# Performance work log

Measured on AMD Instinct MI355X. Metric: run time of the kernel, lower is better.

The kernel has to match this reference:

```python
import jax, jax.numpy as jnp
import numpy as np
import math

E = 8; K = 2; H_FF = 2048; HEADS = 4; COLLAB_STEPS = 2
AUX_W = 0.01; Z_W = 0.001; DROP_W = 0.001; CAP = 1.25; EPS = 1e-6


def _rms(x, w):
    return x * jax.lax.rsqrt(jnp.mean(x * x, -1, keepdims=True) + EPS) * w


def setup_inputs() -> dict:
    key = jax.random.key(0)
    ks = jax.random.split(key, 16)
    D = 768
    f = lambda k, shape: jax.random.normal(k, shape, jnp.float32) * 0.02
    return dict(
        x=jax.random.normal(ks[0], (4, 2048, D), jnp.float32),
        gate_w=f(ks[1], (E, D)),
        w13=f(ks[2], (E, 2 * H_FF, D)),
        w2=f(ks[3], (E, D, H_FF)),
        in_proj_w=f(ks[4], (3 * D, D)),
        in_proj_b=f(ks[5], (3 * D,)),
        out_w=f(ks[6], (D, D)),
        out_b=f(ks[7], (D,)),
        norm1_w=jnp.ones((D,), jnp.float32),
        norm2_w=jnp.ones((D,), jnp.float32),
        ffn_w1=f(ks[8], (D, D)),
        ffn_w2=f(ks[9], (D, D)),
        mediator=f(ks[10], (1, 1, D)),
        fuse_gate_w=f(ks[11], (1, D)),
        fuse_gate_b=jnp.zeros((1,), jnp.float32),
        o_proj_w=f(ks[12], (D, D)),
    )


def reference(x, gate_w, w13, w2, in_proj_w, in_proj_b, out_w, out_b,
              norm1_w, norm2_w, ffn_w1, ffn_w2, mediator,
              fuse_gate_w, fuse_gate_b, o_proj_w):
    B, T, D = x.shape
    N = B * T
    NK = N * K
    xf = x.reshape(N, D).astype(jnp.float32)

    # ---- router (fp32) ----
    logits = xf @ gate_w.T                                  # [N,E]
    topk_vals, topk_idx = jax.lax.top_k(logits, K)          # [N,K]
    topk_probs = jax.nn.softmax(topk_vals, -1)
    router_probs = jax.nn.softmax(logits, -1)
    assign = jnp.zeros((N, E), jnp.float32).at[jnp.arange(N)[:, None], topk_idx].add(topk_probs)
    balance = (router_probs.mean(0) * assign.mean(0)).sum() * E
    z = jax.nn.logsumexp(logits, -1)
    aux = AUX_W * balance + Z_W * (z * z).mean()

    # ---- capacity-limited dispatch (sort by expert, prio-desc within expert) ----
    C = 1 << int(math.ceil(math.log2(math.ceil(NK / E * CAP))))  # static
    x_exp = jnp.repeat(xf, K, axis=0)                       # [NK,D]
    te = topk_idx.reshape(-1)
    prio = topk_vals.reshape(-1)
    order = jnp.lexsort((-prio, te))                        # expert asc, prio desc
    se = te[order]
    counts = jnp.bincount(te, length=E)
    starts = jnp.concatenate([jnp.zeros(1, counts.dtype), jnp.cumsum(counts)[:-1]])
    pos = jnp.arange(NK) - starts[se]                       # rank within expert
    keep_s = pos < C                                        # top-C by router logit kept
    slot = se * C + jnp.minimum(pos, C - 1)
    slot_w = jnp.where(keep_s, slot, E * C)                 # dropped -> scratch row
    buf = jnp.zeros((E * C + 1, D), jnp.float32).at[slot_w].set(x_exp[order])
    buf = buf[:E * C].reshape(E, C, D)

    # ---- experts: ReasoningFeedForward, n_reasoning_steps=1, alpha=1 ----
    gu = jnp.einsum('ecd,ehd->ech', 2.0 * buf, w13)         # [E,C,2H]
    gate_h, up = jnp.split(gu, 2, axis=-1)
    y = buf + jnp.einsum('ech,edh->ecd', jax.nn.silu(gate_h) * up, w2)
    y_flat = y.reshape(E * C, D)
    y_sorted = jnp.where(keep_s[:, None], y_flat[slot], 0.0)
    expert_out = jnp.zeros((NK, D), jnp.float32).at[order].set(y_sorted)
    keep_mask = jnp.zeros((NK,), bool).at[order].set(keep_s)
    aux = aux + DROP_W * (1.0 - keep_s.astype(jnp.float32).mean())  # drop penalty

    km = keep_mask.reshape(N, K)
    expert_states = expert_out.reshape(N, K, D) * km[..., None]
    tp = topk_probs * km
    denom = tp.sum(-1, keepdims=True)
    ok = denom > 0
    weights = jnp.where(ok, tp / jnp.where(ok, denom, 1.0), 0.0)

    # ---- collaboration: mediator token + R rounds of MHA + FFN ----
    tokens = jnp.concatenate([expert_states, jnp.broadcast_to(mediator, (N, 1, D))], 1)  # [N,K+1,D]
    kpm = jnp.concatenate([~km, jnp.zeros((N, 1), bool)], 1)
    bias = jnp.where(kpm, -1e9, 0.0)[:, None, None, :]      # [N,1,1,L]
    dh = D // HEADS
    scale = 1.0 / math.sqrt(dh)
    L = K + 1
    for _ in range(COLLAB_STEPS):
        qkv = tokens @ in_proj_w.T + in_proj_b
        q, k, v = jnp.split(qkv, 3, -1)
        q = q.reshape(N, L, HEADS, dh)
        k = k.reshape(N, L, HEADS, dh)
        v = v.reshape(N, L, HEADS, dh)
        s = jnp.einsum('nqhd,nkhd->nhqk', q, k) * scale + bias
        a = jax.nn.softmax(s, -1)
        o = jnp.einsum('nhqk,nkhd->nqhd', a, v).reshape(N, L, D) @ out_w.T + out_b
        tokens = _rms(tokens + o, norm1_w)
        tokens = tokens + jax.nn.gelu(_rms(tokens, norm2_w) @ ffn_w1.T, approximate=False) @ ffn_w2.T

    med = tokens[:, -1]
    ref = tokens[:, :-1]
    agg = (ref * weights[..., None]).sum(1)
    g = jax.nn.sigmoid(med @ fuse_gate_w.T + fuse_gate_b)   # [N,1]
    fused = (g * med + (1.0 - g) * agg) @ o_proj_w.T
    return fused.reshape(B, T, D), aux, topk_idx.reshape(B, T, K)
```

## Files before the change

### kernel.cpp

```cpp
#include <hip/hip_runtime.h>
#include <math.h>
#include <stdint.h>

#define D_ 768
#define E_ 8
#define K_ 2
#define HFF_ 2048

typedef _Float16 h16;
typedef _Float16 h8 __attribute__((ext_vector_type(8)));
typedef float f32x4 __attribute__((ext_vector_type(4)));

__device__ __forceinline__ float wred(float v){
#pragma unroll
  for (int o = 32; o; o >>= 1) v += __shfl_xor(v, o);
  return v;
}
__device__ __forceinline__ int wredi(int v){
#pragma unroll
  for (int o = 32; o; o >>= 1) v += __shfl_xor(v, o);
  return v;
}
__device__ __forceinline__ float gelu_f(float v){
  return 0.5f * v * (1.f + erff(v * 0.70710678118654752f));
}
__device__ __forceinline__ float silu_f(float v){
  return v / (1.f + expf(-v));
}
__device__ __forceinline__ h8 cvt8(float4 u0, float4 u1, float sc){
  h8 t;
  t[0] = (h16)(u0.x * sc); t[1] = (h16)(u0.y * sc);
  t[2] = (h16)(u0.z * sc); t[3] = (h16)(u0.w * sc);
  t[4] = (h16)(u1.x * sc); t[5] = (h16)(u1.y * sc);
  t[6] = (h16)(u1.z * sc); t[7] = (h16)(u1.w * sc);
  return t;
}
__device__ __forceinline__ void gload16(const h16* g, h16* l){
  __builtin_amdgcn_global_load_lds((const __attribute__((address_space(1))) void*)g,
                                   (__attribute__((address_space(3))) void*)l,
                                   16, 0, 0);
}

__global__ void cvt_k(const float* __restrict__ s, h16* __restrict__ d, int n, float scale)
{
  for (int i = (blockIdx.x * 256 + threadIdx.x) * 4; i < n; i += gridDim.x * 1024) {
    float4 v = *(const float4*)(s + i);
    h16 o0 = (h16)(v.x * scale), o1 = (h16)(v.y * scale);
    h16 o2 = (h16)(v.z * scale), o3 = (h16)(v.w * scale);
    d[i] = o0; d[i + 1] = o1; d[i + 2] = o2; d[i + 3] = o3;
  }
}

__global__ void router_k(const float* __restrict__ x, const float* __restrict__ gw,
                         float* __restrict__ partials, int* __restrict__ pcounts,
                         float* __restrict__ prio, float* __restrict__ tkprob,
                         int* __restrict__ te, float* __restrict__ out_topk, int N)
{
  int wid = threadIdx.x >> 6;
  int lane = threadIdx.x & 63;
  int n = blockIdx.x * 4 + wid;
  __shared__ float lp[4][17];
  __shared__ int lc[4][8];
  float acc[E_];
#pragma unroll
  for (int e = 0; e < E_; e++) acc[e] = 0.f;
  if (n < N) {
    const float* xr = x + (size_t)n * D_;
    for (int c = lane; c < D_; c += 64) {
      float xv = xr[c];
#pragma unroll
      for (int e = 0; e < E_; e++) acc[e] += xv * gw[e * D_ + c];
    }
  }
#pragma unroll
  for (int e = 0; e < E_; e++) acc[e] = wred(acc[e]);
  if (lane == 0) {
    if (n < N) {
      int i0 = 0;
#pragma unroll
      for (int e = 1; e < E_; e++) if (acc[e] > acc[i0]) i0 = e;
      int i1 = -1; float b1 = -3.0e38f;
#pragma unroll
      for (int e = 0; e < E_; e++) if (e != i0 && acc[e] > b1) { b1 = acc[e]; i1 = e; }
      float v0 = acc[i0], v1 = acc[i1];
      float m2 = fmaxf(v0, v1);
      float e0 = expf(v0 - m2), e1 = expf(v1 - m2);
      float p0 = e0 / (e0 + e1), p1 = e1 / (e0 + e1);
      float mx = acc[0];
#pragma unroll
      for (int e = 1; e < E_; e++) mx = fmaxf(mx, acc[e]);
      float se = 0.f;
#pragma unroll
      for (int e = 0; e < E_; e++) se += expf(acc[e] - mx);
      float z = mx + logf(se);
      float inv = 1.f / se;
#pragma unroll
      for (int e = 0; e < E_; e++) lp[wid][e] = expf(acc[e] - mx) * inv;
#pragma unroll
      for (int e = 0; e < E_; e++) lp[wid][8 + e] = (e == i0) ? p0 : ((e == i1) ? p1 : 0.f);
      lp[wid][16] = z * z;
#pragma unroll
      for (int e = 0; e < E_; e++) lc[wid][e] = (e == i0) + (e == i1);
      te[n * 2] = i0; te[n * 2 + 1] = i1;
      prio[n * 2] = v0; prio[n * 2 + 1] = v1;
      tkprob[n * 2] = p0; tkprob[n * 2 + 1] = p1;
      out_topk[n * 2] = (float)i0; out_topk[n * 2 + 1] = (float)i1;
    } else {
      for (int t = 0; t < 17; t++) lp[wid][t] = 0.f;
      for (int e = 0; e < E_; e++) lc[wid][e] = 0;
    }
  }
  __syncthreads();
  int tid = threadIdx.x;
  if (tid < 17)
    partials[(size_t)blockIdx.x * 17 + tid] = lp[0][tid] + lp[1][tid] + lp[2][tid] + lp[3][tid];
  if (tid >= 32 && tid < 40) {
    int e = tid - 32;
    pcounts[(size_t)blockIdx.x * 8 + e] = lc[0][e] + lc[1][e] + lc[2][e] + lc[3][e];
  }
}

__global__ void stats_k(const float* __restrict__ partials, const int* __restrict__ pcounts,
                        int NB, int* __restrict__ counts, int* __restrict__ starts,
                        int* __restrict__ rows_e, int* __restrict__ ctr,
                        float* __restrict__ aux_out, int N, int C)
{
  __shared__ float ssum[17];
  __shared__ int scnt[8];
  int wave = threadIdx.x >> 6, lane = threadIdx.x & 63;
  for (int v = wave; v < 17; v += 4) {
    float s = 0.f;
    for (int b = lane; b < NB; b += 64) s += partials[(size_t)b * 17 + v];
    s = wred(s);
    if (lane == 0) ssum[v] = s;
  }
  for (int e = wave; e < 8; e += 4) {
    int c = 0;
    for (int b = lane; b < NB; b += 64) c += pcounts[(size_t)b * 8 + e];
    c = wredi(c);
    if (lane == 0) scnt[e] = c;
  }
  __syncthreads();
  if (threadIdx.x == 0) {
    int st = 0, kept = 0;
    float bal = 0.f;
    for (int e = 0; e < E_; e++) {
      counts[e] = scnt[e]; starts[e] = st; st += scnt[e];
      int r = scnt[e] < C ? scnt[e] : C;
      rows_e[e] = r; kept += r;
      bal += (ssum[e] / N) * (ssum[8 + e] / N);
      ctr[e] = 0;
    }
    int NK = N * K_;
    float aux = 0.01f * bal * (float)E_ + 0.001f * (ssum[16] / N)
              + 0.001f * (1.f - (float)kept / (float)NK);
    aux_out[0] = aux;
  }
}

__global__ void rank_k(const int* __restrict__ te, const float* __restrict__ prio,
                       const int* __restrict__ counts, const int* __restrict__ starts,
                       int* __restrict__ ctr, int* __restrict__ rowmap,
                       int* __restrict__ keep_nk, int NK, int C)
{
  int i = blockIdx.x * 256 + threadIdx.x;
  if (i >= NK) return;
  int e = te[i];
  int cnt = counts[e];
  int pos;
  if (cnt <= C) {
    pos = atomicAdd(&ctr[e], 1);
  } else {
    float p = prio[i]; int r = 0;
    for (int j = 0; j < NK; j++) {
      if (te[j] == e) { float pj = prio[j]; r += (pj > p) || (pj == p && j < i); }
    }
    pos = r;
  }
  int kp = pos < C ? 1 : 0;
  keep_nk[i] = kp;
  if (kp) rowmap[starts[e] + pos] = i;
}

__global__ void tokinit_k(float* __restrict__ tokens, h16* __restrict__ tokh,
                          const float* __restrict__ med, int total)
{
  for (int idx = blockIdx.x * 256 + threadIdx.x; idx < total; idx += gridDim.x * 256) {
    int r = idx % (3 * D_);
    float v = (r >= 2 * D_) ? med[r - 2 * D_] : 0.f;
    tokens[idx] = v; tokh[idx] = (h16)v;
  }
}

template<int EPI, bool BH>
__global__ __launch_bounds__(256, 2) void mgemm_k(
    const h16* __restrict__ A, int lda, const void* __restrict__ Bv,
    const float* __restrict__ bias, float* C32, h16* C16, int M, int N, int K)
{
  __shared__ __align__(16) h16 ls[16384];
  const int tid = threadIdx.x;
  const int lane = tid & 63, wave = tid >> 6;
  const int wm = wave >> 1, wn = wave & 1;
  const int lr = lane & 15, lk = lane >> 4;
  const int m0 = blockIdx.y * 128, n0 = blockIdx.x * 128;

  f32x4 acc[4][4];
#pragma unroll
  for (int i = 0; i < 4; ++i)
#pragma unroll
    for (int j = 0; j < 4; ++j) acc[i][j] = f32x4{0.f, 0.f, 0.f, 0.f};

  const int ldsbase = (wave < 2) ? wave * 4096 : 8192 + (wave - 2) * 4096;
  const int koff = (wave & 1) * 32 + lk * 8;
  const h16* Bh = (const h16*)Bv;
  const float* Bf = (const float*)Bv;
  size_t srow[8];
  if (wave < 2) {
#pragma unroll
    for (int j = 0; j < 8; ++j) srow[j] = (size_t)(m0 + j * 16 + lr) * (size_t)lda;
  } else {
#pragma unroll
    for (int j = 0; j < 8; ++j) srow[j] = (size_t)(n0 + j * 16 + lr) * (size_t)K;
  }

  const int nkt = K >> 6;
  for (int kt = 0; kt < nkt; ++kt) {
    const int kb = kt * 64 + koff;
    __syncthreads();
    if (wave < 2) {
#pragma unroll
      for (int j = 0; j < 8; ++j) gload16(A + srow[j] + kb, &ls[ldsbase + j * 512]);
    } else if (BH) {
#pragma unroll
      for (int j = 0; j < 8; ++j) gload16(Bh + srow[j] + kb, &ls[ldsbase + j * 512]);
    } else {
#pragma unroll
      for (int j = 0; j < 8; ++j) {
        float4 u0 = *(const float4*)(Bf + srow[j] + kb);
        float4 u1 = *(const float4*)(Bf + srow[j] + kb + 4);
        *(h8*)&ls[ldsbase + j * 512 + lane * 8] = cvt8(u0, u1, 1.f);
      }
    }
    __syncthreads();
#pragma unroll
    for (int kc = 0; kc < 2; ++kc) {
      h8 af[4], bf[4];
#pragma unroll
      for (int i = 0; i < 4; ++i) af[i] = *(const h8*)&ls[(kc * 8 + wm * 4 + i) * 512 + lane * 8];
#pragma unroll
      for (int j = 0; j < 4; ++j) bf[j] = *(const h8*)&ls[8192 + (kc * 8 + wn * 4 + j) * 512 + lane * 8];
#pragma unroll
      for (int i = 0; i < 4; ++i)
#pragma unroll
        for (int j = 0; j < 4; ++j)
          acc[i][j] = __builtin_amdgcn_mfma_f32_16x16x32_f16(af[i], bf[j], acc[i][j], 0, 0, 0);
    }
  }

#pragma unroll
  for (int i = 0; i < 4; ++i) {
    const int row0 = m0 + (wm * 4 + i) * 16 + lk * 4;
#pragma unroll
    for (int j = 0; j < 4; ++j) {
      const int col = n0 + (wn * 4 + j) * 16 + lr;
      const float bv = (EPI == 0 || EPI == 1) ? bias[col] : 0.f;
#pragma unroll
      for (int r = 0; r < 4; ++r) {
        const size_t o = (size_t)(row0 + r) * N + col;
        const float v = acc[i][j][r];
        if (EPI == 0)      { C16[o] = (h16)(v + bv); }
        else if (EPI == 1) { C32[o] += v + bv; }
        else if (EPI == 2) { C16[o] = (h16)gelu_f(v); }
        else if (EPI == 3) { float t = v + C32[o]; C32[o] = t; C16[o] = (h16)t; }
        else               { C32[o] = v; }
      }
    }
  }
}

template<bool BH>
__global__ __launch_bounds__(256, 2) void egemm1_k(
    const float* __restrict__ x, const h16* __restrict__ xh,
    const float* __restrict__ w13, const h16* __restrict__ w13h,
    const int* __restrict__ rowmap, const int* __restrict__ starts,
    const int* __restrict__ rows_e, h16* __restrict__ acth)
{
  const int e = blockIdx.z;
  const int rows = rows_e[e], st = starts[e];
  const int r0 = blockIdx.y * 128;
  if (r0 >= rows) return;
  const int h0 = blockIdx.x * 64;

  __shared__ __align__(16) h16 ls[16384];
  const int tid = threadIdx.x;
  const int lane = tid & 63, wave = tid >> 6;
  const int wm = wave >> 1, wn = wave & 1;
  const int lr = lane & 15, lk = lane >> 4;

  f32x4 acc[4][4];
#pragma unroll
  for (int i = 0; i < 4; ++i)
#pragma unroll
    for (int j = 0; j < 4; ++j) acc[i][j] = f32x4{0.f, 0.f, 0.f, 0.f};

  const int ldsbase = (wave < 2) ? wave * 4096 : 8192 + (wave - 2) * 4096;
  const int koff = (wave & 1) * 32 + lk * 8;
  size_t srow[8];
  if (wave < 2) {
#pragma unroll
    for (int j = 0; j < 8; ++j) {
      int r = r0 + j * 16 + lr; if (r >= rows) r = rows - 1;
      srow[j] = (size_t)(rowmap[st + r] >> 1) * D_;
    }
  } else {
#pragma unroll
    for (int j = 0; j < 8; ++j)
      srow[j] = ((size_t)e * 4096 + (size_t)(j & 1) * 2048 + h0 + (j >> 1) * 16 + lr) * D_;
  }

  for (int kt = 0; kt < D_ / 64; ++kt) {
    const int kb = kt * 64 + koff;
    __syncthreads();
    if (BH) {
      const h16* src = (wave < 2) ? xh : w13h;
#pragma unroll
      for (int j = 0; j < 8; ++j) gload16(src + srow[j] + kb, &ls[ldsbase + j * 512]);
    } else {
      const float* src = (wave < 2) ? x : w13;
      const float sc = (wave < 2) ? 2.f : 1.f;
#pragma unroll
      for (int j = 0; j < 8; ++j) {
        float4 u0 = *(const float4*)(src + srow[j] + kb);
        float4 u1 = *(const float4*)(src + srow[j] + kb + 4);
        *(h8*)&ls[ldsbase + j * 512 + lane * 8] = cvt8(u0, u1, sc);
      }
    }
    __syncthreads();
#pragma unroll
    for (int kc = 0; kc < 2; ++kc) {
      h8 af[4], bf[4];
#pragma unroll
      for (int i = 0; i < 4; ++i) af[i] = *(const h8*)&ls[(kc * 8 + wm * 4 + i) * 512 + lane * 8];
#pragma unroll
      for (int j = 0; j < 4; ++j) bf[j] = *(const h8*)&ls[8192 + (kc * 8 + wn * 4 + j) * 512 + lane * 8];
#pragma unroll
      for (int i = 0; i < 4; ++i)
#pragma unroll
        for (int j = 0; j < 4; ++j)
          acc[i][j] = __builtin_amdgcn_mfma_f32_16x16x32_f16(af[i], bf[j], acc[i][j], 0, 0, 0);
    }
  }

#pragma unroll
  for (int i = 0; i < 4; ++i) {
    const int rloc = r0 + (wm * 4 + i) * 16 + lk * 4;
#pragma unroll
    for (int jc = 0; jc < 2; ++jc) {
      const int col = h0 + (wn * 2 + jc) * 16 + lr;
#pragma unroll
      for (int r = 0; r < 4; ++r) {
        const int rr = rloc + r;
        if (rr < rows) {
          float g = acc[i][2 * jc][r], u = acc[i][2 * jc + 1][r];
          acth[(size_t)(st + rr) * HFF_ + col] = (h16)(silu_f(g) * u);
        }
      }
    }
  }
}

template<bool BH>
__global__ __launch_bounds__(256, 2) void egemm2_k(
    const h16* __restrict__ acth, const float* __restrict__ w2, const h16* __restrict__ w2h,
    const int* __restrict__ rowmap, const int* __restrict__ starts,
    const int* __restrict__ rows_e, const float* __restrict__ x,
    float* __restrict__ tokens, h16* __restrict__ tokh)
{
  const int e = blockIdx.z;
  const int rows = rows_e[e], st = starts[e];
  const int r0 = blockIdx.y * 128;
  if (r0 >= rows) return;
  const int n0 = blockIdx.x * 128;

  __shared__ __align__(16) h16 ls[16384];
  const int tid = threadIdx.x;
  const int lane = tid & 63, wave = tid >> 6;
  const int wm = wave >> 1, wn = wave & 1;
  const int lr = lane & 15, lk = lane >> 4;

  f32x4 acc[4][4];
#pragma unroll
  for (int i = 0; i < 4; ++i)
#pragma unroll
    for (int j = 0; j < 4; ++j) acc[i][j] = f32x4{0.f, 0.f, 0.f, 0.f};

  const int ldsbase = (wave < 2) ? wave * 4096 : 8192 + (wave - 2) * 4096;
  const int koff = (wave & 1) * 32 + lk * 8;
  size_t srow[8];
  if (wave < 2) {
#pragma unroll
    for (int j = 0; j < 8; ++j) {
      int r = r0 + j * 16 + lr; if (r >= rows) r = rows - 1;
      srow[j] = (size_t)(st + r) * HFF_;
    }
  } else {
#pragma unroll
    for (int j = 0; j < 8; ++j)
      srow[j] = ((size_t)e * D_ + n0 + j * 16 + lr) * HFF_;
  }

  for (int kt = 0; kt < HFF_ / 64; ++kt) {
    const int kb = kt * 64 + koff;
    __syncthreads();
    if (wave < 2) {
#pragma unroll
      for (int j = 0; j < 8; ++j) gload16(acth + srow[j] + kb, &ls[ldsbase + j * 512]);
    } else if (BH) {
#pragma unroll
      for (int j = 0; j < 8; ++j) gload16(w2h + srow[j] + kb, &ls[ldsbase + j * 512]);
    } else {
#pragma unroll
      for (int j = 0; j < 8; ++j) {
        float4 u0 = *(const float4*)(w2 + srow[j] + kb);
        float4 u1 = *(const float4*)(w2 + srow[j] + kb + 4);
        *(h8*)&ls[ldsbase + j * 512 + lane * 8] = cvt8(u0, u1, 1.f);
      }
    }
    __syncthreads();
#pragma unroll
    for (int kc = 0; kc < 2; ++kc) {
      h8 af[4], bf[4];
#pragma unroll
      for (int i = 0; i < 4; ++i) af[i] = *(const h8*)&ls[(kc * 8 + wm * 4 + i) * 512 + lane * 8];
#pragma unroll
      for (int j = 0; j < 4; ++j) bf[j] = *(const h8*)&ls[8192 + (kc * 8 + wn * 4 + j) * 512 + lane * 8];
#pragma unroll
      for (int i = 0; i < 4; ++i)
#pragma unroll
        for (int j = 0; j < 4; ++j)
          acc[i][j] = __builtin_amdgcn_mfma_f32_16x16x32_f16(af[i], bf[j], acc[i][j], 0, 0, 0);
    }
  }

#pragma unroll
  for (int i = 0; i < 4; ++i) {
    const int rloc = r0 + (wm * 4 + i) * 16 + lk * 4;
#pragma unroll
    for (int j = 0; j < 4; ++j) {
      const int col = n0 + (wn * 4 + j) * 16 + lr;
#pragma unroll
      for (int r = 0; r < 4; ++r) {
        const int rr = rloc + r;
        if (rr < rows) {
          int item = rowmap[st + rr];
          int t = item >> 1, l = item & 1;
          size_t o = ((size_t)t * 3 + l) * D_ + col;
          float v = acc[i][j][r] + x[(size_t)t * D_ + col];
          tokens[o] = v; tokh[o] = (h16)v;
        }
      }
    }
  }
}

__global__ void attn_k(h16* qkv, const int* __restrict__ keep_nk, int N)
{
  int n = blockIdx.x;
  int h = threadIdx.y, lane = threadIdx.x;
  h16* base = qkv + (size_t)n * 3 * 2304;
  float qr[3][3], kr[3][3], vr[3][3];
#pragma unroll
  for (int l2 = 0; l2 < 3; l2++) {
    const h16* row = base + l2 * 2304 + h * 192;
#pragma unroll
    for (int c = 0; c < 3; c++) {
      qr[l2][c] = (float)row[c * 64 + lane];
      kr[l2][c] = (float)row[768 + c * 64 + lane];
      vr[l2][c] = (float)row[1536 + c * 64 + lane];
    }
  }
  const float scale = 0.07216878364870323f;
  float bj0 = keep_nk[n * 2] ? 0.f : -1e9f;
  float bj1 = keep_nk[n * 2 + 1] ? 0.f : -1e9f;
  float a[3][3];
#pragma unroll
  for (int i2 = 0; i2 < 3; i2++) {
    float s0 = wred(qr[i2][0] * kr[0][0] + qr[i2][1] * kr[0][1] + qr[i2][2] * kr[0][2]) * scale + bj0;
    float s1 = wred(qr[i2][0] * kr[1][0] + qr[i2][1] * kr[1][1] + qr[i2][2] * kr[1][2]) * scale + bj1;
    float s2 = wred(qr[i2][0] * kr[2][0] + qr[i2][1] * kr[2][1] + qr[i2][2] * kr[2][2]) * scale;
    float m = fmaxf(s0, fmaxf(s1, s2));
    float e0 = expf(s0 - m), e1 = expf(s1 - m), e2 = expf(s2 - m);
    float inv = 1.f / (e0 + e1 + e2);
    a[i2][0] = e0 * inv; a[i2][1] = e1 * inv; a[i2][2] = e2 * inv;
  }
#pragma unroll
  for (int i2 = 0; i2 < 3; i2++) {
    h16* dst = base + i2 * 2304 + h * 192;
#pragma unroll
    for (int c = 0; c < 3; c++)
      dst[c * 64 + lane] = (h16)(a[i2][0] * vr[0][c] + a[i2][1] * vr[1][c] + a[i2][2] * vr[2][c]);
  }
}

__global__ void rms12_k(float* tokens, const float* __restrict__ w1,
                        const float* __restrict__ w2, h16* __restrict__ nrmh)
{
  int row = blockIdx.x, tid = threadIdx.x;
  float* s = tokens + (size_t)row * D_;
  float v0 = s[tid], v1 = s[tid + 256], v2 = s[tid + 512];
  __shared__ float redA[4], redB[4];
  float ss = v0 * v0 + v1 * v1 + v2 * v2;
  float wsum = wred(ss);
  if ((tid & 63) == 0) redA[tid >> 6] = wsum;
  __syncthreads();
  float tot = redA[0] + redA[1] + redA[2] + redA[3];
  float r = 1.f / sqrtf(tot * (1.f / 768.f) + 1e-6f);
  float t0 = v0 * r * w1[tid];
  float t1 = v1 * r * w1[tid + 256];
  float t2 = v2 * r * w1[tid + 512];
  float ss2 = t0 * t0 + t1 * t1 + t2 * t2;
  float wsum2 = wred(ss2);
  if ((tid & 63) == 0) redB[tid >> 6] = wsum2;
  __syncthreads();
  float tot2 = redB[0] + redB[1] + redB[2] + redB[3];
  float r2 = 1.f / sqrtf(tot2 * (1.f / 768.f) + 1e-6f);
  s[tid] = t0; s[tid + 256] = t1; s[tid + 512] = t2;
  h16* dd = nrmh + (size_t)row * D_;
  dd[tid]       = (h16)(t0 * r2 * w2[tid]);
  dd[tid + 256] = (h16)(t1 * r2 * w2[tid + 256]);
  dd[tid + 512] = (h16)(t2 * r2 * w2[tid + 512]);
}

__global__ void fuse_k(const float* __restrict__ tokens, const float* __restrict__ tkprob,
                       const int* __restrict__ keep_nk, const float* __restrict__ fw,
                       const float* __restrict__ fb, h16* __restrict__ out)
{
  int n = blockIdx.x; int tid = threadIdx.x;
  const float* t0 = tokens + ((size_t)n * 3 + 0) * D_;
  const float* t1 = tokens + ((size_t)n * 3 + 1) * D_;
  const float* md = tokens + ((size_t)n * 3 + 2) * D_;
  float p = md[tid] * fw[tid] + md[tid + 256] * fw[tid + 256] + md[tid + 512] * fw[tid + 512];
  __shared__ float red[4];
  float wsum = wred(p);
  if ((tid & 63) == 0) red[tid >> 6] = wsum;
  __syncthreads();
  float dot = red[0] + red[1] + red[2] + red[3];
  float g = 1.f / (1.f + expf(-(dot + fb[0])));
  float tp0 = keep_nk[n * 2] ? tkprob[n * 2] : 0.f;
  float tp1 = keep_nk[n * 2 + 1] ? tkprob[n * 2 + 1] : 0.f;
  float den = tp0 + tp1;
  float w0 = den > 0.f ? tp0 / den : 0.f;
  float w1 = den > 0.f ? tp1 / den : 0.f;
  h16* d = out + (size_t)n * D_;
#pragma unroll
  for (int c3 = 0; c3 < 3; c3++) {
    int c = tid + c3 * 256;
    d[c] = (h16)(g * md[c] + (1.f - g) * (w0 * t0[c] + w1 * t1[c]));
  }
}

template<bool BH>
static void run_pipeline(const float* x, const float* gate_w, const float* w13,
                         const float* w2, const float* in_proj_w, const float* in_proj_b,
                         const float* out_w, const float* out_b, const float* norm1_w,
                         const float* norm2_w, const float* ffn_w1, const float* ffn_w2,
                         const float* mediator, const float* fuse_w, const float* fuse_b,
                         const float* o_proj_w,
                         float* partials, int* pcounts, int* counts, int* starts,
                         int* rows_e, int* ctr, int* te, int* keep_nk, int* rowmap,
                         float* prio, float* tkprob, float* tokens, h16* tokh, h16* big,
                         h16* xh, h16* w13h, h16* w2h, h16* inprojh, h16* outwh,
                         h16* ffn1h, h16* ffn2h, h16* oprojh,
                         float* out_fused, float* out_aux, float* out_topk,
                         int N, int C, int NB, int M3, hipStream_t stream)
{
  h16* acth   = big;
  h16* qkvh   = big;
  h16* nrmh   = big;
  h16* h1h    = big + (size_t)M3 * D_;
  h16* fusedh = big;

  if (BH) {
    cvt_k<<<512,  256, 0, stream>>>(x, xh, N * D_, 1.0f);
    cvt_k<<<2048, 256, 0, stream>>>(w13, w13h, E_ * 2 * HFF_ * D_, 2.0f);
    cvt_k<<<2048, 256, 0, stream>>>(w2, w2h, E_ * D_ * HFF_, 1.0f);
    cvt_k<<<256,  256, 0, stream>>>(in_proj_w, inprojh, 3 * D_ * D_, 1.0f);
    cvt_k<<<128,  256, 0, stream>>>(out_w, outwh, D_ * D_, 1.0f);
    cvt_k<<<128,  256, 0, stream>>>(ffn_w1, ffn1h, D_ * D_, 1.0f);
    cvt_k<<<128,  256, 0, stream>>>(ffn_w2, ffn2h, D_ * D_, 1.0f);
    cvt_k<<<128,  256, 0, stream>>>(o_proj_w, oprojh, D_ * D_, 1.0f);
  }

  router_k<<<NB, 256, 0, stream>>>(x, gate_w, partials, pcounts, prio, tkprob, te, out_topk, N);
  stats_k<<<1, 256, 0, stream>>>(partials, pcounts, NB, counts, starts, rows_e, ctr, out_aux, N, C);
  rank_k<<<(N * K_ + 255) / 256, 256, 0, stream>>>(te, prio, counts, starts, ctr, rowmap, keep_nk, N * K_, C);
  tokinit_k<<<2048, 256, 0, stream>>>(tokens, tokh, mediator, M3 * D_);

  int ytil = (C + 127) / 128;
  egemm1_k<BH><<<dim3(HFF_ / 64, ytil, E_), 256, 0, stream>>>(x, xh, w13, w13h, rowmap, starts, rows_e, acth);
  egemm2_k<BH><<<dim3(D_ / 128, ytil, E_), 256, 0, stream>>>(acth, w2, w2h, rowmap, starts, rows_e, x, tokens, tokh);

  const void* inpB  = BH ? (const void*)inprojh : (const void*)in_proj_w;
  const void* outB  = BH ? (const void*)outwh   : (const void*)out_w;
  const void* f1B   = BH ? (const void*)ffn1h   : (const void*)ffn_w1;
  const void* f2B   = BH ? (const void*)ffn2h   : (const void*)ffn_w2;
  const void* opB   = BH ? (const void*)oprojh  : (const void*)o_proj_w;

  for (int step = 0; step < 2; step++) {
    mgemm_k<0, BH><<<dim3(2304 / 128, M3 / 128), 256, 0, stream>>>(tokh, D_, inpB, in_proj_b, nullptr, qkvh, M3, 2304, D_);
    attn_k<<<N, dim3(64, 4), 0, stream>>>(qkvh, keep_nk, N);
    mgemm_k<1, BH><<<dim3(D_ / 128, M3 / 128), 256, 0, stream>>>(qkvh, 2304, outB, out_b, tokens, nullptr, M3, D_, D_);
    rms12_k<<<M3, 256, 0, stream>>>(tokens, norm1_w, norm2_w, nrmh);
    mgemm_k<2, BH><<<dim3(D_ / 128, M3 / 128), 256, 0, stream>>>(nrmh, D_, f1B, nullptr, nullptr, h1h, M3, D_, D_);
    mgemm_k<3, BH><<<dim3(D_ / 128, M3 / 128), 256, 0, stream>>>(h1h, D_, f2B, nullptr, tokens, tokh, M3, D_, D_);
  }

  fuse_k<<<N, 256, 0, stream>>>(tokens, tkprob, keep_nk, fuse_w, fuse_b, fusedh);
  mgemm_k<4, BH><<<dim3(D_ / 128, N / 128), 256, 0, stream>>>(fusedh, D_, opB, nullptr, out_fused, nullptr, N, D_, D_);
}

extern "C" void kernel_launch(void* const* d_in, const int* in_sizes, int n_in,
                              void* d_out, int out_size, void* d_ws, size_t ws_size,
                              hipStream_t stream) {
  const float* x         = (const float*)d_in[0];
  const float* gate_w    = (const float*)d_in[1];
  const float* w13       = (const float*)d_in[2];
  const float* w2        = (const float*)d_in[3];
  const float* in_proj_w = (const float*)d_in[4];
  const float* in_proj_b = (const float*)d_in[5];
  const float* out_w     = (const float*)d_in[6];
  const float* out_b     = (const float*)d_in[7];
  const float* norm1_w   = (const float*)d_in[8];
  const float* norm2_w   = (const float*)d_in[9];
  const float* ffn_w1    = (const float*)d_in[10];
  const float* ffn_w2    = (const float*)d_in[11];
  const float* mediator  = (const float*)d_in[12];
  const float* fuse_w    = (const float*)d_in[13];
  const float* fuse_b    = (const float*)d_in[14];
  const float* o_proj_w  = (const float*)d_in[15];

  const int N = in_sizes[0] / D_;
  const int NK = N * K_;
  int capc = (int)ceil((double)NK / E_ * 1.25);
  int C = 1; while (C < capc) C <<= 1;
  const int NB = (N + 3) / 4;
  const int M3 = N * 3;

  size_t off = 0;
  auto alloc = [&](size_t bytes) -> void* {
    void* r = (char*)d_ws + off;
    off += (bytes + 255) & ~(size_t)255;
    return r;
  };
  float* partials = (float*)alloc(sizeof(float) * (size_t)NB * 17);
  int*   pcounts  = (int*)alloc(sizeof(int) * (size_t)NB * 8);
  int*   counts   = (int*)alloc(sizeof(int) * 8);
  int*   starts   = (int*)alloc(sizeof(int) * 8);
  int*   rows_e   = (int*)alloc(sizeof(int) * 8);
  int*   ctr      = (int*)alloc(sizeof(int) * 8);
  int*   te       = (int*)alloc(sizeof(int) * (size_t)NK);
  int*   keep_nk  = (int*)alloc(sizeof(int) * (size_t)NK);
  int*   rowmap   = (int*)alloc(sizeof(int) * (size_t)NK);
  float* prio     = (float*)alloc(sizeof(float) * (size_t)NK);
  float* tkprob   = (float*)alloc(sizeof(float) * (size_t)NK);
  float* tokens   = (float*)alloc(sizeof(float) * (size_t)M3 * D_);
  h16*   tokh     = (h16*)alloc(sizeof(h16) * (size_t)M3 * D_);
  h16*   big      = (h16*)alloc(sizeof(h16) * (size_t)M3 * 2304);
  h16* xh      = (h16*)alloc(sizeof(h16) * (size_t)N * D_);
  h16* w13h    = (h16*)alloc(sizeof(h16) * (size_t)E_ * 2 * HFF_ * D_);
  h16* w2h     = (h16*)alloc(sizeof(h16) * (size_t)E_ * D_ * HFF_);
  h16* inprojh = (h16*)alloc(sizeof(h16) * (size_t)3 * D_ * D_);
  h16* outwh   = (h16*)alloc(sizeof(h16) * (size_t)D_ * D_);
  h16* ffn1h   = (h16*)alloc(sizeof(h16) * (size_t)D_ * D_);
  h16* ffn2h   = (h16*)alloc(sizeof(h16) * (size_t)D_ * D_);
  h16* oprojh  = (h16*)alloc(sizeof(h16) * (size_t)D_ * D_);
  const bool use_bh = (off <= ws_size);

  float* out_fused = (float*)d_out;
  float* out_aux   = out_fused + (size_t)N * D_;
  float* out_topk  = out_aux + 1;

  if (use_bh)
    run_pipeline<true>(x, gate_w, w13, w2, in_proj_w, in_proj_b, out_w, out_b, norm1_w,
                       norm2_w, ffn_w1, ffn_w2, mediator, fuse_w, fuse_b, o_proj_w,
                       partials, pcounts, counts, starts, rows_e, ctr, te, keep_nk, rowmap,
                       prio, tkprob, tokens, tokh, big, xh, w13h, w2h, inprojh, outwh,
                       ffn1h, ffn2h, oprojh, out_fused, out_aux, out_topk,
                       N, C, NB, M3, stream);
  else
    run_pipeline<false>(x, gate_w, w13, w2, in_proj_w, in_proj_b, out_w, out_b, norm1_w,
                        norm2_w, ffn_w1, ffn_w2, mediator, fuse_w, fuse_b, o_proj_w,
                        partials, pcounts, counts, starts, rows_e, ctr, te, keep_nk, rowmap,
                        prio, tkprob, tokens, tokh, big, xh, w13h, w2h, inprojh, outwh,
                        ffn1h, ffn2h, oprojh, out_fused, out_aux, out_topk,
                        N, C, NB, M3, stream);
}
```

Measured before the change: 1.843 ms.

## Double-buffer LDS in fp16 GEMM kernels with async global-to-LDS prefetch

Adds a shared mfma_core routine that splits the 16K-half LDS buffer into two stages with a K-step of 32. It prefetches the next tile with global_load_lds while running MFMAs on the current one, using explicit vmcnt waits and s_barrier in place of the two __syncthreads per tile. This applies to the dense GEMM and both expert GEMMs whenever the weights are already fp16. The aim is to hide global load latency behind compute. The cost is twice as many barriers per unit of K and less data loaded per stage.

```diff
diff --git a/kernel.cpp b/kernel.cpp
--- a/kernel.cpp
+++ b/kernel.cpp
@@ -39,6 +39,54 @@
   __builtin_amdgcn_global_load_lds((const __attribute__((address_space(1))) void*)g,
                                    (__attribute__((address_space(3))) void*)l,
                                    16, 0, 0);
+}
+
+__device__ __forceinline__ void mfma_core(const h16* __restrict__ src,
+    const size_t* srow, int nkt, h16* ls, f32x4 (&acc)[4][4], int lane, int wave)
+{
+  const int wm = wave >> 1, wn = wave & 1;
+  const int lk8 = (lane >> 4) * 8;
+  const int ub0 = ((wave >= 2) ? 4096 : 0) + (wave & 1) * 2048;
+
+  {
+    const h16* s0 = src + lk8;
+#pragma unroll
+    for (int j = 0; j < 4; ++j)
+      gload16(s0 + srow[j], &ls[ub0 + j * 512]);
+  }
+  for (int kt = 0; kt < nkt; ++kt) {
+    const int sel = kt & 1;
+    if (kt + 1 < nkt) {
+      const h16* s0 = src + (kt + 1) * 32 + lk8;
+      const int db = (sel ^ 1) * 8192 + ub0;
+#pragma unroll
+      for (int j = 0; j < 4; ++j)
+        gload16(s0 + srow[j], &ls[db + j * 512]);
+      __builtin_amdgcn_sched_barrier(0);
+      asm volatile("s_waitcnt vmcnt(4)" ::: "memory");
+    } else {
+      __builtin_amdgcn_sched_barrier(0);
+      asm volatile("s_waitcnt vmcnt(0)" ::: "memory");
+    }
+    __builtin_amdgcn_sched_barrier(0);
+    __builtin_amdgcn_s_barrier();
+    __builtin_amdgcn_sched_barrier(0);
+    const int ab = sel * 8192 + wm * 2048 + lane * 8;
+    const int bb = sel * 8192 + 4096 + wn * 2048 + lane * 8;
+    h8 af[4], bf[4];
+#pragma unroll
+    for (int i = 0; i < 4; ++i) af[i] = *(const h8*)&ls[ab + i * 512];
+#pragma unroll
+    for (int j = 0; j < 4; ++j) bf[j] = *(const h8*)&ls[bb + j * 512];
+#pragma unroll
+    for (int i = 0; i < 4; ++i)
+#pragma unroll
+      for (int j = 0; j < 4; ++j)
+        acc[i][j] = __builtin_amdgcn_mfma_f32_16x16x32_f16(af[i], bf[j], acc[i][j], 0, 0, 0);
+    __builtin_amdgcn_sched_barrier(0);
+    __builtin_amdgcn_s_barrier();
+    __builtin_amdgcn_sched_barrier(0);
+  }
 }
 
 __global__ void cvt_k(const float* __restrict__ s, h16* __restrict__ d, int n, float scale)
@@ -210,50 +258,63 @@
 #pragma unroll
     for (int j = 0; j < 4; ++j) acc[i][j] = f32x4{0.f, 0.f, 0.f, 0.f};
 
-  const int ldsbase = (wave < 2) ? wave * 4096 : 8192 + (wave - 2) * 4096;
-  const int koff = (wave & 1) * 32 + lk * 8;
-  const h16* Bh = (const h16*)Bv;
-  const float* Bf = (const float*)Bv;
-  size_t srow[8];
-  if (wave < 2) {
-#pragma unroll
-    for (int j = 0; j < 8; ++j) srow[j] = (size_t)(m0 + j * 16 + lr) * (size_t)lda;
+  if constexpr (BH) {
+    const h16* Bh = (const h16*)Bv;
+    size_t srow[4];
+    const h16* src;
+    if (wave < 2) {
+#pragma unroll
+      for (int j = 0; j < 4; ++j)
+        srow[j] = (size_t)(m0 + ((wave & 1) * 4 + j) * 16 + lr) * (size_t)lda;
+      src = A;
+    } else {
+#pragma unroll
+      for (int j = 0; j < 4; ++j)
+        srow[j] = (size_t)(n0 + ((wave & 1) * 4 + j) * 16 + lr) * (size_t)K;
+      src = Bh;
+    }
+    mfma_core(src, srow, K >> 5, ls, acc, lane, wave);
   } else {
-#pragma unroll
-    for (int j = 0; j < 8; ++j) srow[j] = (size_t)(n0 + j * 16 + lr) * (size_t)K;
-  }
-
-  const int nkt = K >> 6;
-  for (int kt = 0; kt < nkt; ++kt) {
-    const int kb = kt * 64 + koff;
-    __syncthreads();
+    const float* Bf = (const float*)Bv;
+    const int ldsbase = (wave < 2) ? wave * 4096 : 8192 + (wave - 2) * 4096;
+    const int koff = (wave & 1) * 32 + lk * 8;
+    size_t srow[8];
     if (wave < 2) {
 #pragma unroll
-      for (int j = 0; j < 8; ++j) gload16(A + srow[j] + kb, &ls[ldsbase + j * 512]);
-    } else if (BH) {
-#pragma unroll
-      for (int j = 0; j < 8; ++j) gload16(Bh + srow[j] + kb, &ls[ldsbase + j * 512]);
+      for (int j = 0; j < 8; ++j) srow[j] = (size_t)(m0 + j * 16 + lr) * (size_t)lda;
     } else {
 #pragma unroll
-      for (int j = 0; j < 8; ++j) {
-        float4 u0 = *(const float4*)(Bf + srow[j] + kb);
-        float4 u1 = *(const float4*)(Bf + srow[j] + kb + 4);
-        *(h8*)&ls[ldsbase + j * 512 + lane * 8] = cvt8(u0, u1, 1.f);
-      }
-    }
-    __syncthreads();
-#pragma unroll
-    for (int kc = 0; kc < 2; ++kc) {
-      h8 af[4], bf[4];
-#pragma unroll
-      for (int i = 0; i < 4; ++i) af[i] = *(const h8*)&ls[(kc * 8 + wm * 4 + i) * 512 + lane * 8];
-#pragma unroll
-      for (int j = 0; j < 4; ++j) bf[j] = *(const h8*)&ls[8192 + (kc * 8 + wn * 4 + j) * 512 + lane * 8];
-#pragma unroll
-      for (int i = 0; i < 4; ++i)
-#pragma unroll
-        for (int j = 0; j < 4; ++j)
-          acc[i][j] = __builtin_amdgcn_mfma_f32_16x16x32_f16(af[i], bf[j], acc[i][j], 0, 0, 0);
+      for (int j = 0; j < 8; ++j) srow[j] = (size_t)(n0 + j * 16 + lr) * (size_t)K;
+    }
+    const int nkt = K >> 6;
+    for (int kt = 0; kt < nkt; ++kt) {
+      const int kb = kt * 64 + koff;
+      __syncthreads();
+      if (wave < 2) {
+#pragma unroll
+        for (int j = 0; j < 8; ++j) gload16(A + srow[j] + kb, &ls[ldsbase + j * 512]);
+      } else {
+#pragma unroll
+        for (int j = 0; j < 8; ++j) {
+          float4 u0 = *(const float4*)(Bf + srow[j] + kb);
+          float4 u1 = *(const float4*)(Bf + srow[j] + kb + 4);
+          *(h8*)&ls[ldsbase + j * 512 + lane * 8] = cvt8(u0, u1, 1.f);
+        }
+      }
+      __syncthreads();
+#pragma unroll
+      for (int kc = 0; kc < 2; ++kc) {
+        h8 af[4], bf[4];
+#pragma unroll
+        for (int i = 0; i < 4; ++i) af[i] = *(const h8*)&ls[(kc * 8 + wm * 4 + i) * 512 + lane * 8];
+#pragma unroll
+        for (int j = 0; j < 4; ++j) bf[j] = *(const h8*)&ls[8192 + (kc * 8 + wn * 4 + j) * 512 + lane * 8];
+#pragma unroll
+        for (int i = 0; i < 4; ++i)
+#pragma unroll
+          for (int j = 0; j < 4; ++j)
+            acc[i][j] = __builtin_amdgcn_mfma_f32_16x16x32_f16(af[i], bf[j], acc[i][j], 0, 0, 0);
+      }
     }
   }
 
@@ -303,29 +364,43 @@
 #pragma unroll
     for (int j = 0; j < 4; ++j) acc[i][j] = f32x4{0.f, 0.f, 0.f, 0.f};
 
-  const int ldsbase = (wave < 2) ? wave * 4096 : 8192 + (wave - 2) * 4096;
-  const int koff = (wave & 1) * 32 + lk * 8;
-  size_t srow[8];
-  if (wave < 2) {
-#pragma unroll
-    for (int j = 0; j < 8; ++j) {
-      int r = r0 + j * 16 + lr; if (r >= rows) r = rows - 1;
-      srow[j] = (size_t)(rowmap[st + r] >> 1) * D_;
-    }
+  if constexpr (BH) {
+    size_t srow[4];
+    const h16* src;
+    if (wave < 2) {
+#pragma unroll
+      for (int j = 0; j < 4; ++j) {
+        int r = r0 + ((wave & 1) * 4 + j) * 16 + lr; if (r >= rows) r = rows - 1;
+        srow[j] = (size_t)(rowmap[st + r] >> 1) * D_;
+      }
+      src = xh;
+    } else {
+#pragma unroll
+      for (int j = 0; j < 4; ++j) {
+        int u = (wave & 1) * 4 + j;
+        srow[j] = ((size_t)e * 4096 + (size_t)(u & 1) * 2048 + h0 + (u >> 1) * 16 + lr) * D_;
+      }
+      src = w13h;
+    }
+    mfma_core(src, srow, D_ / 32, ls, acc, lane, wave);
   } else {
-#pragma unroll
-    for (int j = 0; j < 8; ++j)
-      srow[j] = ((size_t)e * 4096 + (size_t)(j & 1) * 2048 + h0 + (j >> 1) * 16 + lr) * D_;
-  }
-
-  for (int kt = 0; kt < D_ / 64; ++kt) {
-    const int kb = kt * 64 + koff;
-    __syncthreads();
-    if (BH) {
-      const h16* src = (wave < 2) ? xh : w13h;
-#pragma unroll
-      for (int j = 0; j < 8; ++j) gload16(src + srow[j] + kb, &ls[ldsbase + j * 512]);
+    const int ldsbase = (wave < 2) ? wave * 4096 : 8192 + (wave - 2) * 4096;
+    const int koff = (wave & 1) * 32 + lk * 8;
+    size_t srow[8];
+    if (wave < 2) {
+#pragma unroll
+      for (int j = 0; j < 8; ++j) {
+        int r = r0 + j * 16 + lr; if (r >= rows) r = rows - 1;
+        srow[j] = (size_t)(rowmap[st + r] >> 1) * D_;
+      }
     } else {
+#pragma unroll
+      for (int j = 0; j < 8; ++j)
+        srow[j] = ((size_t)e * 4096 + (size_t)(j & 1) * 2048 + h0 + (j >> 1) * 16 + lr) * D_;
+    }
+    for (int kt = 0; kt < D_ / 64; ++kt) {
+      const int kb = kt * 64 + koff;
+      __syncthreads();
       const float* src = (wave < 2) ? x : w13;
       const float sc = (wave < 2) ? 2.f : 1.f;
 #pragma unroll
@@ -334,20 +409,20 @@
         float4 u1 = *(const float4*)(src + srow[j] + kb + 4);
         *(h8*)&ls[ldsbase + j * 512 + lane * 8] = cvt8(u0, u1, sc);
       }
-    }
-    __syncthreads();
-#pragma unroll
-    for (int kc = 0; kc < 2; ++kc) {
-      h8 af[4], bf[4];
-#pragma unroll
-      for (int i = 0; i < 4; ++i) af[i] = *(const h8*)&ls[(kc * 8 + wm * 4 + i) * 512 + lane * 8];
-#pragma unroll
-      for (int j = 0; j < 4; ++j) bf[j] = *(const h8*)&ls[8192 + (kc * 8 + wn * 4 + j) * 512 + lane * 8];
-#pragma unroll
-      for (int i = 0; i < 4; ++i)
-#pragma unroll
-        for (int j = 0; j < 4; ++j)
-          acc[i][j] = __builtin_amdgcn_mfma_f32_16x16x32_f16(af[i], bf[j], acc[i][j], 0, 0, 0);
+      __syncthreads();
+#pragma unroll
+      for (int kc = 0; kc < 2; ++kc) {
+        h8 af[4], bf[4];
+#pragma unroll
+        for (int i = 0; i < 4; ++i) af[i] = *(const h8*)&ls[(kc * 8 + wm * 4 + i) * 512 + lane * 8];
+#pragma unroll
+        for (int j = 0; j < 4; ++j) bf[j] = *(const h8*)&ls[8192 + (kc * 8 + wn * 4 + j) * 512 + lane * 8];
+#pragma unroll
+        for (int i = 0; i < 4; ++i)
+#pragma unroll
+          for (int j = 0; j < 4; ++j)
+            acc[i][j] = __builtin_amdgcn_mfma_f32_16x16x32_f16(af[i], bf[j], acc[i][j], 0, 0, 0);
+      }
     }
   }
 
@@ -394,51 +469,66 @@
 #pragma unroll
     for (int j = 0; j < 4; ++j) acc[i][j] = f32x4{0.f, 0.f, 0.f, 0.f};
 
-  const int ldsbase = (wave < 2) ? wave * 4096 : 8192 + (wave - 2) * 4096;
-  const int koff = (wave & 1) * 32 + lk * 8;
-  size_t srow[8];
-  if (wave < 2) {
-#pragma unroll
-    for (int j = 0; j < 8; ++j) {
-      int r = r0 + j * 16 + lr; if (r >= rows) r = rows - 1;
-      srow[j] = (size_t)(st + r) * HFF_;
-    }
+  if constexpr (BH) {
+    size_t srow[4];
+    const h16* src;
+    if (wave < 2) {
+#pragma unroll
+      for (int j = 0; j < 4; ++j) {
+        int r = r0 + ((wave & 1) * 4 + j) * 16 + lr; if (r >= rows) r = rows - 1;
+        srow[j] = (size_t)(st + r) * HFF_;
+      }
+      src = acth;
+    } else {
+#pragma unroll
+      for (int j = 0; j < 4; ++j)
+        srow[j] = ((size_t)e * D_ + n0 + ((wave & 1) * 4 + j) * 16 + lr) * HFF_;
+      src = w2h;
+    }
+    mfma_core(src, srow, HFF_ / 32, ls, acc, lane, wave);
   } else {
-#pragma unroll
-    for (int j = 0; j < 8; ++j)
-      srow[j] = ((size_t)e * D_ + n0 + j * 16 + lr) * HFF_;
-  }
-
-  for (int kt = 0; kt < HFF_ / 64; ++kt) {
-    const int kb = kt * 64 + koff;
-    __syncthreads();
+    const int ldsbase = (wave < 2) ? wave * 4096 : 8192 + (wave - 2) * 4096;
+    const int koff = (wave & 1) * 32 + lk * 8;
+    size_t srow[8];
     if (wave < 2) {
 #pragma unroll
-      for (int j = 0; j < 8; ++j) gload16(acth + srow[j] + kb, &ls[ldsbase + j * 512]);
-    } else if (BH) {
-#pragma unroll
-      for (int j = 0; j < 8; ++j) gload16(w2h + srow[j] + kb, &ls[ldsbase + j * 512]);
+      for (int j = 0; j < 8; ++j) {
+        int r = r0 + j * 16 + lr; if (r >= rows) r = rows - 1;
+        srow[j] = (size_t)(st + r) * HFF_;
+      }
     } else {
 #pragma unroll
-      for (int j = 0; j < 8; ++j) {
-        float4 u0 = *(const float4*)(w2 + srow[j] + kb);
-        float4 u1 = *(const float4*)(w2 + srow[j] + kb + 4);
-        *(h8*)&ls[ldsbase + j * 512 + lane * 8] = cvt8(u0, u1, 1.f);
-      }
-    }
-    __syncthreads();
-#pragma unroll
-    for (int kc = 0; kc < 2; ++kc) {
-      h8 af[4], bf[4];
-#pragma unroll
-      for (int i = 0; i < 4; ++i) af[i] = *(const h8*)&ls[(kc * 8 + wm * 4 + i) * 512 + lane * 8];
-#pragma unroll
-      for (int j = 0; j < 4; ++j) bf[j] = *(const h8*)&ls[8192 + (kc * 8 + wn * 4 + j) * 512 + lane * 8];
-#pragma unroll
-      for (int i = 0; i < 4; ++i)
-#pragma unroll
-        for (int j = 0; j < 4; ++j)
-          acc[i][j] = __builtin_amdgcn_mfma_f32_16x16x32_f16(af[i], bf[j], acc[i][j], 0, 0, 0);
+      for (int j = 0; j < 8; ++j)
+        srow[j] = ((size_t)e * D_ + n0 + j * 16 + lr) * HFF_;
+    }
+    for (int kt = 0; kt < HFF_ / 64; ++kt) {
+      const int kb = kt * 64 + koff;
+      __syncthreads();
+      if (wave < 2) {
+#pragma unroll
+        for (int j = 0; j < 8; ++j) gload16(acth + srow[j] + kb, &ls[ldsbase + j * 512]);
+      } else {
+#pragma unroll
+        for (int j = 0; j < 8; ++j) {
+          float4 u0 = *(const float4*)(w2 + srow[j] + kb);
+          float4 u1 = *(const float4*)(w2 + srow[j] + kb + 4);
+          *(h8*)&ls[ldsbase + j * 512 + lane * 8] = cvt8(u0, u1, 1.f);
+        }
+      }
+      __syncthreads();
+#pragma unroll
+      for (int kc = 0; kc < 2; ++kc) {
+        h8 af[4], bf[4];
+#pragma unroll
+        for (int i = 0; i < 4; ++i) af[i] = *(const h8*)&ls[(kc * 8 + wm * 4 + i) * 512 + lane * 8];
+#pragma unroll
+        for (int j = 0; j < 4; ++j) bf[j] = *(const h8*)&ls[8192 + (kc * 8 + wn * 4 + j) * 512 + lane * 8];
+#pragma unroll
+        for (int i = 0; i < 4; ++i)
+#pragma unroll
+          for (int j = 0; j < 4; ++j)
+            acc[i][j] = __builtin_amdgcn_mfma_f32_16x16x32_f16(af[i], bf[j], acc[i][j], 0, 0, 0);
+      }
     }
   }
 
```

New measurement: 1.786 ms. -3.1%, faster.
